# Kernel tuning notes

Hardware: AMD Instinct MI355X
Metric: run time of the kernel (lower is better)

The kernel has to match this reference:

```python
import jax, jax.numpy as jnp
import numpy as np

B, N, D = 16, 4096, 1024
G = 64  # number of groups
TEMPERATURE = 0.1


def _build_indices(seed=0):
    """Replicates the torch module's per-group sampling deterministically on host."""
    rng = np.random.default_rng(seed)
    flat_groups = rng.integers(0, G, size=B * N)
    all_idx = np.arange(B * N)
    anchors, positives, negatives = [], [], []
    for g in range(G):
        idxs = all_idx[flat_groups == g]
        if idxs.size < 2:
            continue
        perm = rng.permutation(idxs)
        pos = np.roll(perm, 1)
        comp = all_idx[flat_groups != g]
        if comp.size == 0:
            continue
        neg = comp[rng.integers(0, comp.size, size=idxs.size)]
        anchors.append(perm)
        positives.append(pos)
        negatives.append(neg)
    return (np.concatenate(anchors), np.concatenate(positives), np.concatenate(negatives))


def setup_inputs() -> dict:
    key = jax.random.key(0)
    embeddings = jax.random.normal(key, (B, N, D), dtype=jnp.float32)
    a, p, n = _build_indices(seed=0)
    return {
        "embeddings": embeddings,
        "anchor_idx": jnp.asarray(a, dtype=jnp.int64) if jax.config.jax_enable_x64 else jnp.asarray(a, dtype=jnp.int32),
        "pos_idx": jnp.asarray(p, dtype=jnp.int32),
        "neg_idx": jnp.asarray(n, dtype=jnp.int32),
    }


def reference(embeddings, anchor_idx, pos_idx, neg_idx):
    b, n, d = embeddings.shape
    flat = embeddings.reshape(b * n, d)                      # [BN, D]
    a = flat[anchor_idx]                                     # [A, D]
    p = flat[pos_idx]                                        # [A, D]
    ng = flat[neg_idx]                                       # [A, D]
    pos_score = jnp.sum(a * p, axis=1) / TEMPERATURE         # [A]
    neg_score = jnp.sum(a * ng, axis=1) / TEMPERATURE        # [A]
    # CrossEntropy with label 0 over 2-way logits [pos, neg]:
    # loss_i = logsumexp([pos_i, neg_i]) - pos_i  (numerically stable)
    logits = jnp.stack([pos_score, neg_score], axis=1)       # [A, 2]
    loss = jnp.mean(jax.nn.logsumexp(logits, axis=1) - pos_score)
    return loss
```

## Files before the change

kernel.cpp:

```cpp
#include <hip/hip_runtime.h>
#include <math.h>


#define EMB_D 1024
#define TEMP_INV 10.0f
#define NBLOCKS 2048
#define NTHREADS 256
#define WAVES_PER_BLOCK (NTHREADS / 64)

__global__ __launch_bounds__(NTHREADS) void infonce_partial_kernel(
    const float* __restrict__ emb,
    const int* __restrict__ anchor_idx,
    const int* __restrict__ pos_idx,
    const int* __restrict__ neg_idx,
    float* __restrict__ ws_partial,
    int A)
{
    __shared__ float wave_sums[WAVES_PER_BLOCK];

    const int tid  = threadIdx.x;
    const int lane = tid & 63;
    const int wid  = tid >> 6;
    const int gwave  = blockIdx.x * WAVES_PER_BLOCK + wid;
    const int nwaves = gridDim.x * WAVES_PER_BLOCK;

    float loss_sum = 0.0f;

    for (int a = gwave; a < A; a += nwaves) {
        const float4* ar = (const float4*)(emb + (size_t)anchor_idx[a] * EMB_D);
        const float4* pr = (const float4*)(emb + (size_t)pos_idx[a]    * EMB_D);
        const float4* nr = (const float4*)(emb + (size_t)neg_idx[a]    * EMB_D);

        float dp = 0.0f, dn = 0.0f;
        #pragma unroll
        for (int it = 0; it < EMB_D / 4 / 64; ++it) {
            const int j = lane + it * 64;
            const float4 av = ar[j];
            const float4 pv = pr[j];
            const float4 nv = nr[j];
            dp = fmaf(av.x, pv.x, dp);
            dp = fmaf(av.y, pv.y, dp);
            dp = fmaf(av.z, pv.z, dp);
            dp = fmaf(av.w, pv.w, dp);
            dn = fmaf(av.x, nv.x, dn);
            dn = fmaf(av.y, nv.y, dn);
            dn = fmaf(av.z, nv.z, dn);
            dn = fmaf(av.w, nv.w, dn);
        }

        #pragma unroll
        for (int off = 32; off >= 1; off >>= 1) {
            dp += __shfl_xor(dp, off, 64);
            dn += __shfl_xor(dn, off, 64);
        }

        const float d = (dn - dp) * TEMP_INV;
        const float loss = (d > 0.0f) ? (d + log1pf(__expf(-d)))
                                      : log1pf(__expf(d));
        loss_sum += loss;
    }

    if (lane == 0) wave_sums[wid] = loss_sum;
    __syncthreads();

    if (tid == 0) {
        float s = 0.0f;
        #pragma unroll
        for (int i = 0; i < WAVES_PER_BLOCK; ++i) s += wave_sums[i];
        ws_partial[blockIdx.x] = s;
    }
}

__global__ __launch_bounds__(256) void infonce_reduce_kernel(
    const float* __restrict__ ws_partial,
    float* __restrict__ out,
    int nparts,
    float invA)
{
    __shared__ double sh[256];
    double s = 0.0;
    for (int i = threadIdx.x; i < nparts; i += 256) s += (double)ws_partial[i];
    sh[threadIdx.x] = s;
    __syncthreads();
    #pragma unroll
    for (int off = 128; off >= 1; off >>= 1) {
        if (threadIdx.x < off) sh[threadIdx.x] += sh[threadIdx.x + off];
        __syncthreads();
    }
    if (threadIdx.x == 0) out[0] = (float)(sh[0] * (double)invA);
}

extern "C" void kernel_launch(void* const* d_in, const int* in_sizes, int n_in,
                              void* d_out, int out_size, void* d_ws, size_t ws_size,
                              hipStream_t stream) {
    const float* emb        = (const float*)d_in[0];
    const int*   anchor_idx = (const int*)d_in[1];
    const int*   pos_idx    = (const int*)d_in[2];
    const int*   neg_idx    = (const int*)d_in[3];
    const int    A          = in_sizes[1];

    float* ws  = (float*)d_ws;
    float* out = (float*)d_out;

    infonce_partial_kernel<<<NBLOCKS, NTHREADS, 0, stream>>>(
        emb, anchor_idx, pos_idx, neg_idx, ws, A);
    infonce_reduce_kernel<<<1, 256, 0, stream>>>(
        ws, out, NBLOCKS, 1.0f / (float)A);
}
```

Baseline: 97.35 us.

## Reuse previous anchor row as positive via contiguous per-wave chunks

Each wave now processes a contiguous chunk of anchor entries instead of a strided set. When the current positive index equals the previous anchor index, the anchor row already held in registers is reused rather than reloaded from memory. This targets the gather bandwidth cost by removing most positive-row loads. The trade-offs are an index comparison and held registers, and the benefit depends on how the positive indices are laid out.

```diff
diff --git a/kernel.cpp b/kernel.cpp
--- a/kernel.cpp
+++ b/kernel.cpp
@@ -7,6 +7,14 @@
 #define NBLOCKS 2048
 #define NTHREADS 256
 #define WAVES_PER_BLOCK (NTHREADS / 64)
+
+__device__ __forceinline__ float dot4(const float4 a, const float4 b, float acc) {
+    acc = fmaf(a.x, b.x, acc);
+    acc = fmaf(a.y, b.y, acc);
+    acc = fmaf(a.z, b.z, acc);
+    acc = fmaf(a.w, b.w, acc);
+    return acc;
+}
 
 __global__ __launch_bounds__(NTHREADS) void infonce_partial_kernel(
     const float* __restrict__ emb,
@@ -22,31 +30,51 @@
     const int lane = tid & 63;
     const int wid  = tid >> 6;
     const int gwave  = blockIdx.x * WAVES_PER_BLOCK + wid;
-    const int nwaves = gridDim.x * WAVES_PER_BLOCK;
+    const int nwaves = NBLOCKS * WAVES_PER_BLOCK;
+
+    const int chunk = (A + nwaves - 1) / nwaves;
+    const int a0 = gwave * chunk;
+    const int a1 = (a0 + chunk < A) ? (a0 + chunk) : A;
 
     float loss_sum = 0.0f;
 
-    for (int a = gwave; a < A; a += nwaves) {
-        const float4* ar = (const float4*)(emb + (size_t)anchor_idx[a] * EMB_D);
-        const float4* pr = (const float4*)(emb + (size_t)pos_idx[a]    * EMB_D);
-        const float4* nr = (const float4*)(emb + (size_t)neg_idx[a]    * EMB_D);
+    int prev_ai = -1;
+    float4 pv[4];
+    pv[0] = pv[1] = pv[2] = pv[3] = make_float4(0.f, 0.f, 0.f, 0.f);
+
+    for (int a = a0; a < a1; ++a) {
+        const int ai = anchor_idx[a];
+        const int pi = pos_idx[a];
+        const int ni = neg_idx[a];
+
+        const float4* ar = (const float4*)(emb + (size_t)ai * EMB_D);
+        const float4* nr = (const float4*)(emb + (size_t)ni * EMB_D);
+
+        float4 av[4], nv[4];
+        #pragma unroll
+        for (int it = 0; it < 4; ++it) {
+            av[it] = ar[lane + it * 64];
+            nv[it] = nr[lane + it * 64];
+        }
 
         float dp = 0.0f, dn = 0.0f;
+        if (pi == prev_ai) {
+            #pragma unroll
+            for (int it = 0; it < 4; ++it) dp = dot4(av[it], pv[it], dp);
+        } else {
+            const float4* pr = (const float4*)(emb + (size_t)pi * EMB_D);
+            #pragma unroll
+            for (int it = 0; it < 4; ++it) {
+                const float4 t = pr[lane + it * 64];
+                dp = dot4(av[it], t, dp);
+            }
+        }
         #pragma unroll
-        for (int it = 0; it < EMB_D / 4 / 64; ++it) {
-            const int j = lane + it * 64;
-            const float4 av = ar[j];
-            const float4 pv = pr[j];
-            const float4 nv = nr[j];
-            dp = fmaf(av.x, pv.x, dp);
-            dp = fmaf(av.y, pv.y, dp);
-            dp = fmaf(av.z, pv.z, dp);
-            dp = fmaf(av.w, pv.w, dp);
-            dn = fmaf(av.x, nv.x, dn);
-            dn = fmaf(av.y, nv.y, dn);
-            dn = fmaf(av.z, nv.z, dn);
-            dn = fmaf(av.w, nv.w, dn);
-        }
+        for (int it = 0; it < 4; ++it) dn = dot4(av[it], nv[it], dn);
+
+        #pragma unroll
+        for (int it = 0; it < 4; ++it) pv[it] = av[it];
+        prev_ai = ai;
 
         #pragma unroll
         for (int off = 32; off >= 1; off >>= 1) {
```

After: 90.65 us. -6.9%, faster.
